# Kernel optimization log

Hardware: AMD Instinct MI355X
Metric: run time of the kernel (lower is better)

Reference implementation:

```python
import jax, jax.numpy as jnp
import numpy as np

N = 50000      # nodes
E = 640000     # edges (before self-loops)
FIN = 512      # in_channels
H = 4          # heads
C = 32         # per-head dim (hidden_channels // heads)
HID = 128      # hidden_channels
OUT = 64       # out_channels
NC = 2         # num_classes


def setup_inputs() -> dict:
    key = jax.random.key(0)
    ks = jax.random.split(key, 26)
    rn = lambda k, shp, s=0.05: jax.random.normal(k, shp, jnp.float32) * s
    return {
        "x": jax.random.normal(ks[0], (N, FIN), jnp.float32),
        "edge_index": jax.random.randint(ks[1], (2, E), 0, N, dtype=jnp.int32),
        "batch": jnp.zeros((N,), jnp.int32),
        # GATConv 1: FIN -> H x C (concat -> HID)
        "W1": rn(ks[2], (FIN, H * C)), "as1": rn(ks[3], (H, C)), "ad1": rn(ks[4], (H, C)), "b1": jnp.zeros((H * C,), jnp.float32),
        "g1": jnp.ones((HID,), jnp.float32), "be1": jnp.zeros((HID,), jnp.float32),
        # GATConv 2: HID -> H x C
        "W2": rn(ks[5], (HID, H * C)), "as2": rn(ks[6], (H, C)), "ad2": rn(ks[7], (H, C)), "b2": jnp.zeros((H * C,), jnp.float32),
        "g2": jnp.ones((HID,), jnp.float32), "be2": jnp.zeros((HID,), jnp.float32),
        "W3": rn(ks[8], (HID, OUT)), "as3": rn(ks[9], (1, OUT)), "ad3": rn(ks[10], (1, OUT)), "b3": jnp.zeros((OUT,), jnp.float32),
        "g3": jnp.ones((OUT,), jnp.float32), "be3": jnp.zeros((OUT,), jnp.float32),
        # classifier: Linear(2*OUT, HID) -> ReLU -> Linear(HID, NC)
        "cW1": rn(ks[11], (2 * OUT, HID)), "cb1": jnp.zeros((HID,), jnp.float32),
        "cW2": rn(ks[12], (HID, NC)), "cb2": jnp.zeros((NC,), jnp.float32),
    }


def _gat_conv(x, ei, W, a_s, a_d, b, heads, cdim, concat):
    n = x.shape[0]
    h = (x @ W).reshape(n, heads, cdim)                 # [n,H,C]
    src, dst = ei[0], ei[1]
    al_s = (h * a_s).sum(-1)                            # [n,H]
    al_d = (h * a_d).sum(-1)                            # [n,H]
    e = al_s[src] + al_d[dst]                           # [E',H]
    e = jnp.where(e > 0, e, 0.2 * e)                    # LeakyReLU(0.2)
    m = jax.ops.segment_max(e, dst, num_segments=n)     # segment softmax over dst
    ex = jnp.exp(e - m[dst])
    s = jax.ops.segment_sum(ex, dst, num_segments=n)
    alpha = ex / (s[dst] + 1e-16)                       # [E',H]
    out = jax.ops.segment_sum(h[src] * alpha[:, :, None], dst, num_segments=n)
    out = out.reshape(n, heads * cdim) if concat else out.mean(axis=1)
    return out + b


def _layer_norm(x, g, b):
    mu = x.mean(-1, keepdims=True)
    v = ((x - mu) ** 2).mean(-1, keepdims=True)
    return g * (x - mu) * jax.lax.rsqrt(v + 1e-5) + b


def reference(x, edge_index, batch, W1, as1, ad1, b1, g1, be1, W2, as2, ad2, b2, g2, be2, W3, as3, ad3, b3, g3, be3, cW1, cb1, cW2, cb2):
    n = x.shape[0]
    ar = jnp.arange(n, dtype=edge_index.dtype)
    ei = jnp.concatenate([edge_index, jnp.stack([ar, ar])], axis=1)  # add self-loops (PyG default)
    h = jax.nn.elu(_layer_norm(_gat_conv(x, ei, W1, as1, ad1, b1, H, C, True), g1, be1))
    h = jax.nn.elu(_layer_norm(_gat_conv(h, ei, W2, as2, ad2, b2, H, C, True), g2, be2))
    h = jax.nn.elu(_layer_norm(_gat_conv(h, ei, W3, as3, ad3, b3, 1, OUT, False), g3, be3))
    # global mean / max pooling over batch ids (single graph here, B=1)
    B = 1
    cnt = jax.ops.segment_sum(jnp.ones((n, 1), h.dtype), batch, num_segments=B)
    x_mean = jax.ops.segment_sum(h, batch, num_segments=B) / cnt
    x_max = jax.ops.segment_max(h, batch, num_segments=B)
    z = jnp.concatenate([x_mean, x_max], axis=-1)       # [B, 2*OUT]
    z = jax.nn.relu(z @ cW1 + cb1)
    return z @ cW2 + cb2                                 # [B, NC]
```

## Files before the change

kernel.cpp:

```cpp
#include <hip/hip_runtime.h>
#include <cmath>

static constexpr int TPB = 256;

using short8 = __attribute__((ext_vector_type(8))) short;
using half8  = __attribute__((ext_vector_type(8))) _Float16;
using f32x4  = __attribute__((ext_vector_type(4))) float;
using uint4v = __attribute__((ext_vector_type(4))) unsigned int;
typedef unsigned short ushort;
typedef unsigned int uint;

__device__ __forceinline__ ushort f2h(float f) {
  _Float16 h = (_Float16)f;
  return __builtin_bit_cast(ushort, h);
}
__device__ __forceinline__ float h2f(ushort u) {
  return (float)__builtin_bit_cast(_Float16, u);
}
__device__ __forceinline__ float hlo(uint u) { return h2f((ushort)(u & 0xffffu)); }
__device__ __forceinline__ float hhi(uint u) { return h2f((ushort)(u >> 16)); }

__global__ void prep_wt3(const float* __restrict__ W1, ushort* __restrict__ Wt1,
                         const float* __restrict__ W2, ushort* __restrict__ Wt2,
                         const float* __restrict__ W3, ushort* __restrict__ Wt3,
                         int FIN) {
  int idx = blockIdx.x * TPB + threadIdx.x;
  const int n1 = FIN * 128, n2 = 128 * 128, n3 = 128 * 64;
  if (idx < n1) {
    int nc = idx / FIN, k = idx - nc * FIN;
    Wt1[idx] = f2h(W1[(size_t)k * 128 + nc]);
  } else if (idx < n1 + n2) {
    int i = idx - n1;
    int nc = i / 128, k = i - nc * 128;
    Wt2[i] = f2h(W2[(size_t)k * 128 + nc]);
  } else if (idx < n1 + n2 + n3) {
    int i = idx - n1 - n2;
    int nc = i / 128, k = i - nc * 128;
    Wt3[i] = f2h(W3[(size_t)k * 64 + nc]);
  }
}

template <int ABF16, int BN, int FUSEMODE>
__global__ __launch_bounds__(256) void gemm_mfma(const void* __restrict__ Ap,
                                                 const ushort* __restrict__ Wt,
                                                 ushort* __restrict__ Cb,
                                                 int n, int K,
                                                 const float* __restrict__ a_s,
                                                 const float* __restrict__ a_d,
                                                 float* __restrict__ als,
                                                 float* __restrict__ ald) {
  constexpr int NF = BN / 32;
  __shared__ short As[64 * 72];
  __shared__ short Bs[BN * 72];
  const int tid = threadIdx.x;
  const int row0 = blockIdx.x * 64;
  const int srow = tid >> 2, sks = (tid & 3) << 4;
  const int wave = tid >> 6, lane = tid & 63;
  const int wr = wave >> 1, wc = wave & 1;
  const int lm = lane & 15, lg = lane >> 4;

  f32x4 acc[2][NF] = {};

  for (int k0 = 0; k0 < K; k0 += 64) {
    {
      int gr = row0 + srow;
      short8 v0 = {0, 0, 0, 0, 0, 0, 0, 0}, v1 = v0;
      if constexpr (ABF16 == 0) {
        const float* A = (const float*)Ap;
        if (gr < n) {
          const float* p = A + (size_t)gr * K + k0 + sks;
          float4 f0 = *(const float4*)(p + 0);
          float4 f1 = *(const float4*)(p + 4);
          float4 f2 = *(const float4*)(p + 8);
          float4 f3 = *(const float4*)(p + 12);
          v0[0] = (short)f2h(f0.x); v0[1] = (short)f2h(f0.y); v0[2] = (short)f2h(f0.z); v0[3] = (short)f2h(f0.w);
          v0[4] = (short)f2h(f1.x); v0[5] = (short)f2h(f1.y); v0[6] = (short)f2h(f1.z); v0[7] = (short)f2h(f1.w);
          v1[0] = (short)f2h(f2.x); v1[1] = (short)f2h(f2.y); v1[2] = (short)f2h(f2.z); v1[3] = (short)f2h(f2.w);
          v1[4] = (short)f2h(f3.x); v1[5] = (short)f2h(f3.y); v1[6] = (short)f2h(f3.z); v1[7] = (short)f2h(f3.w);
        }
      } else {
        const ushort* A = (const ushort*)Ap;
        if (gr < n) {
          const ushort* p = A + (size_t)gr * K + k0 + sks;
          v0 = *(const short8*)(p + 0);
          v1 = *(const short8*)(p + 8);
        }
      }
      *(short8*)&As[srow * 72 + sks + 0] = v0;
      *(short8*)&As[srow * 72 + sks + 8] = v1;
    }
    if constexpr (BN == 128) {
      const int brow = tid >> 1, bks = (tid & 1) << 5;
      const ushort* wp = Wt + (size_t)brow * K + k0 + bks;
      *(short8*)&Bs[brow * 72 + bks + 0]  = *(const short8*)(wp + 0);
      *(short8*)&Bs[brow * 72 + bks + 8]  = *(const short8*)(wp + 8);
      *(short8*)&Bs[brow * 72 + bks + 16] = *(const short8*)(wp + 16);
      *(short8*)&Bs[brow * 72 + bks + 24] = *(const short8*)(wp + 24);
    } else {
      const ushort* wp = Wt + (size_t)srow * K + k0 + sks;
      *(short8*)&Bs[srow * 72 + sks + 0] = *(const short8*)(wp + 0);
      *(short8*)&Bs[srow * 72 + sks + 8] = *(const short8*)(wp + 8);
    }
    __syncthreads();
#pragma unroll
    for (int kk = 0; kk < 64; kk += 32) {
      half8 a0 = *(const half8*)&As[(wr * 32 + lm) * 72 + kk + lg * 8];
      half8 a1 = *(const half8*)&As[(wr * 32 + 16 + lm) * 72 + kk + lg * 8];
      half8 bf[NF];
#pragma unroll
      for (int f = 0; f < NF; ++f)
        bf[f] = *(const half8*)&Bs[(wc * (BN / 2) + f * 16 + lm) * 72 + kk + lg * 8];
#pragma unroll
      for (int f = 0; f < NF; ++f) {
        acc[0][f] = __builtin_amdgcn_mfma_f32_16x16x32_f16(a0, bf[f], acc[0][f], 0, 0, 0);
        acc[1][f] = __builtin_amdgcn_mfma_f32_16x16x32_f16(a1, bf[f], acc[1][f], 0, 0, 0);
      }
    }
    __syncthreads();
  }
#pragma unroll
  for (int m = 0; m < 2; ++m)
#pragma unroll
    for (int f = 0; f < NF; ++f)
#pragma unroll
      for (int r = 0; r < 4; ++r) {
        int row = row0 + wr * 32 + m * 16 + lg * 4 + r;
        if (row < n) {
          int col = wc * (BN / 2) + f * 16 + lm;
          Cb[(size_t)row * BN + col] = f2h(acc[m][f][r]);
        }
      }
  if constexpr (FUSEMODE == 1) {
#pragma unroll
    for (int hh = 0; hh < 2; ++hh) {
      const int head = 2 * wc + hh;
      float as0 = a_s[head * 32 + lm], as1 = a_s[head * 32 + 16 + lm];
      float ad0 = a_d[head * 32 + lm], ad1 = a_d[head * 32 + 16 + lm];
#pragma unroll
      for (int m = 0; m < 2; ++m)
#pragma unroll
        for (int r = 0; r < 4; ++r) {
          float tS = acc[m][2 * hh][r] * as0 + acc[m][2 * hh + 1][r] * as1;
          float tD = acc[m][2 * hh][r] * ad0 + acc[m][2 * hh + 1][r] * ad1;
#pragma unroll
          for (int off = 8; off >= 1; off >>= 1) {
            tS += __shfl_xor(tS, off);
            tD += __shfl_xor(tD, off);
          }
          if (lm == 0) {
            int row = row0 + wr * 32 + m * 16 + lg * 4 + r;
            if (row < n) {
              als[(size_t)row * 4 + head] = tS;
              ald[(size_t)row * 4 + head] = tD;
            }
          }
        }
    }
  }
  if constexpr (FUSEMODE == 2) {
    float* alsp = (float*)As;
    float* aldp = alsp + 64;
    float tS[2][4], tD[2][4];
#pragma unroll
    for (int m = 0; m < 2; ++m)
#pragma unroll
      for (int r = 0; r < 4; ++r) {
        int col0c = wc * 32;
        float s = acc[m][0][r] * a_s[col0c + lm] + acc[m][1][r] * a_s[col0c + 16 + lm];
        float dd = acc[m][0][r] * a_d[col0c + lm] + acc[m][1][r] * a_d[col0c + 16 + lm];
#pragma unroll
        for (int off = 8; off >= 1; off >>= 1) {
          s += __shfl_xor(s, off);
          dd += __shfl_xor(dd, off);
        }
        tS[m][r] = s;
        tD[m][r] = dd;
      }
    if (wc == 0) {
#pragma unroll
      for (int m = 0; m < 2; ++m)
#pragma unroll
        for (int r = 0; r < 4; ++r)
          if (lm == 0) {
            int rl = wr * 32 + m * 16 + lg * 4 + r;
            alsp[rl] = tS[m][r];
            aldp[rl] = tD[m][r];
          }
    }
    __syncthreads();
    if (wc == 1) {
#pragma unroll
      for (int m = 0; m < 2; ++m)
#pragma unroll
        for (int r = 0; r < 4; ++r)
          if (lm == 0) {
            int rl = wr * 32 + m * 16 + lg * 4 + r;
            int row = row0 + rl;
            if (row < n) {
              als[row] = alsp[rl] + tS[m][r];
              ald[row] = aldp[rl] + tD[m][r];
            }
          }
    }
  }
}

__global__ void zero_int(int* __restrict__ p, int n) {
  int i = blockIdx.x * TPB + threadIdx.x;
  if (i < n) p[i] = 0;
}

__global__ void hist_dst(const int* __restrict__ edst, int* __restrict__ counts,
                         int E0, int Et) {
  int e = blockIdx.x * TPB + threadIdx.x;
  if (e >= Et) return;
  int d = e < E0 ? edst[e] : e - E0;
  atomicAdd(&counts[d], 1);
}

__global__ void block_sums(const int* __restrict__ counts, int* __restrict__ bsum, int N) {
  __shared__ int sh[256];
  int t = threadIdx.x, idx = blockIdx.x * 256 + t;
  sh[t] = idx < N ? counts[idx] : 0;
  __syncthreads();
  for (int off = 128; off >= 1; off >>= 1) {
    if (t < off) sh[t] += sh[t + off];
    __syncthreads();
  }
  if (t == 0) bsum[blockIdx.x] = sh[0];
}

__global__ void scan_bsum(int* __restrict__ bsum, int nb) {
  __shared__ int sh[256];
  int t = threadIdx.x;
  int v = t < nb ? bsum[t] : 0;
  sh[t] = v;
  __syncthreads();
  for (int off = 1; off < 256; off <<= 1) {
    int u = (t >= off) ? sh[t - off] : 0;
    __syncthreads();
    sh[t] += u;
    __syncthreads();
  }
  if (t < nb) bsum[t] = sh[t] - v;
}

__global__ void scan_final(const int* __restrict__ counts, const int* __restrict__ bsum_ex,
                           int* __restrict__ offsets, int* __restrict__ cursor,
                           int N, int Et) {
  __shared__ int sh[256];
  int t = threadIdx.x, b = blockIdx.x;
  int idx = b * 256 + t;
  int v = (idx < N) ? counts[idx] : 0;
  sh[t] = v;
  __syncthreads();
  for (int off = 1; off < 256; off <<= 1) {
    int u = (t >= off) ? sh[t - off] : 0;
    __syncthreads();
    sh[t] += u;
    __syncthreads();
  }
  if (idx < N) {
    int o = bsum_ex[b] + sh[t] - v;
    offsets[idx] = o;
    cursor[idx] = o;
  }
  if (idx == 0) offsets[N] = Et;
}

__global__ void scatter_csr(const int* __restrict__ esrc, const int* __restrict__ edst,
                            int* __restrict__ cursor, int* __restrict__ csr_src,
                            int E0, int Et) {
  int e = blockIdx.x * TPB + threadIdx.x;
  if (e >= Et) return;
  int s = e < E0 ? esrc[e] : e - E0;
  int d = e < E0 ? edst[e] : e - E0;
  int pos = atomicAdd(&cursor[d], 1);
  csr_src[pos] = s;
}

template <int HH, int CC>
__global__ __launch_bounds__(256) void fused_attn(
    const ushort* __restrict__ hb, const float* __restrict__ als,
    const float* __restrict__ ald, const int* __restrict__ offsets,
    const int* __restrict__ csr_src, const float* __restrict__ bias,
    const float* __restrict__ g, const float* __restrict__ be,
    ushort* __restrict__ xout, int n) {
  constexpr int W = HH * CC;
  constexpr int LPE = W / 8;
  constexpr int NEG = 64 / LPE;
  int wid = (int)((blockIdx.x * (size_t)blockDim.x + threadIdx.x) >> 6);
  int lane = threadIdx.x & 63;
  if (wid >= n) return;
  const int d = wid;
  const int begin = offsets[d], end = offsets[d + 1];
  const int deg = end - begin;

  const int grp = lane / LPE, sub = lane % LPE;
  const int c0 = sub * 8;

  float acc[8] = {};

  if (HH == 4 && deg <= 16) {
    const int h16 = lane >> 4, j16 = lane & 15;
    bool act = j16 < deg;
    int s_e = csr_src[begin + (act ? j16 : 0)];
    float e;
    {
      float ad_h = ald[(size_t)d * 4 + h16];
      e = act ? (als[(size_t)s_e * 4 + h16] + ad_h) : -1e30f;
      e = e > 0.f ? e : 0.2f * e;
    }
    float m = e;
#pragma unroll
    for (int off = 8; off >= 1; off >>= 1) m = fmaxf(m, __shfl_xor(m, off));
    float p = act ? __expf(e - m) : 0.f;
    float s = p;
#pragma unroll
    for (int off = 8; off >= 1; off >>= 1) s += __shfl_xor(s, off);
    float alpha = p / (s + 1e-16f);

    const int hc = sub >> 2;
    int j = grp;
    int sj = __shfl(s_e, j & 15);
    uint4v u = *(const uint4v*)(hb + (size_t)sj * W + c0);
    for (int j0 = 0; j0 < deg; j0 += NEG) {
      uint4v ucur = u;
      int jcur = j;
      j += NEG;
      if (j0 + NEG < deg) {
        int sn = __shfl(s_e, j & 15);
        u = *(const uint4v*)(hb + (size_t)sn * W + c0);
      }
      float w = __shfl(alpha, (hc << 4) | (jcur & 15));
#pragma unroll
      for (int i = 0; i < 4; ++i) {
        acc[2 * i]     = fmaf(w, hlo(ucur[i]), acc[2 * i]);
        acc[2 * i + 1] = fmaf(w, hhi(ucur[i]), acc[2 * i + 1]);
      }
    }
  } else {

  const int hsel = sub >> 2;
  float aldv[HH];
  if constexpr (HH == 4) {
    float4 t = *(const float4*)(ald + (size_t)d * 4);
    aldv[0] = t.x; aldv[1] = t.y; aldv[2] = t.z; aldv[3] = t.w;
  } else {
    aldv[0] = ald[d];
  }

  auto sel4 = [&](float x0, float x1, float x2, float x3) {
    float lo = (hsel & 1) ? x1 : x0;
    float hi = (hsel & 1) ? x3 : x2;
    return (hsel & 2) ? hi : lo;
  };

  if (deg <= 64) {
    bool act = lane < deg;
    int s_e = act ? csr_src[begin + lane] : 0;
    float e0 = -1e30f, e1 = -1e30f, e2 = -1e30f, e3 = -1e30f;
    if constexpr (HH == 4) {
      if (act) {
        float4 t = *(const float4*)(als + (size_t)s_e * 4);
        e0 = t.x + aldv[0]; e0 = e0 > 0.f ? e0 : 0.2f * e0;
        e1 = t.y + aldv[1]; e1 = e1 > 0.f ? e1 : 0.2f * e1;
        e2 = t.z + aldv[2]; e2 = e2 > 0.f ? e2 : 0.2f * e2;
        e3 = t.w + aldv[3]; e3 = e3 > 0.f ? e3 : 0.2f * e3;
      }
    } else {
      if (act) {
        e0 = als[s_e] + aldv[0]; e0 = e0 > 0.f ? e0 : 0.2f * e0;
      }
    }
    float m0 = e0, m1 = e1, m2 = e2, m3 = e3;
#pragma unroll
    for (int off = 32; off >= 1; off >>= 1) {
      m0 = fmaxf(m0, __shfl_xor(m0, off));
      if constexpr (HH == 4) {
        m1 = fmaxf(m1, __shfl_xor(m1, off));
        m2 = fmaxf(m2, __shfl_xor(m2, off));
        m3 = fmaxf(m3, __shfl_xor(m3, off));
      }
    }
    float p0 = act ? __expf(e0 - m0) : 0.f;
    float p1 = 0.f, p2 = 0.f, p3 = 0.f;
    if constexpr (HH == 4) {
      p1 = act ? __expf(e1 - m1) : 0.f;
      p2 = act ? __expf(e2 - m2) : 0.f;
      p3 = act ? __expf(e3 - m3) : 0.f;
    }
    float s0 = p0, s1 = p1, s2 = p2, s3 = p3;
#pragma unroll
    for (int off = 32; off >= 1; off >>= 1) {
      s0 += __shfl_xor(s0, off);
      if constexpr (HH == 4) {
        s1 += __shfl_xor(s1, off);
        s2 += __shfl_xor(s2, off);
        s3 += __shfl_xor(s3, off);
      }
    }
    float a0 = p0 / (s0 + 1e-16f);
    float a1 = 0.f, a2 = 0.f, a3 = 0.f;
    if constexpr (HH == 4) {
      a1 = p1 / (s1 + 1e-16f);
      a2 = p2 / (s2 + 1e-16f);
      a3 = p3 / (s3 + 1e-16f);
    }

    int j = grp;
    int sj = __shfl(s_e, j < 64 ? j : 0);
    uint4v u = *(const uint4v*)(hb + (size_t)sj * W + c0);
    for (int j0 = 0; j0 < deg; j0 += NEG) {
      uint4v ucur = u;
      int jcur = j;
      j += NEG;
      if (j0 + NEG < deg) {
        int sn = __shfl(s_e, j < 64 ? j : 0);
        u = *(const uint4v*)(hb + (size_t)sn * W + c0);
      }
      int jc = jcur < 64 ? jcur : 0;
      float w;
      if constexpr (HH == 4) {
        float wa = __shfl(a0, jc), wb = __shfl(a1, jc), wcx = __shfl(a2, jc), wd = __shfl(a3, jc);
        w = sel4(wa, wb, wcx, wd);
      } else {
        w = __shfl(a0, jc);
      }
      if (jcur >= deg) w = 0.f;
#pragma unroll
      for (int i = 0; i < 4; ++i) {
        acc[2 * i]     = fmaf(w, hlo(ucur[i]), acc[2 * i]);
        acc[2 * i + 1] = fmaf(w, hhi(ucur[i]), acc[2 * i + 1]);
      }
    }
  } else {
    float me[HH];
#pragma unroll
    for (int h = 0; h < HH; ++h) me[h] = -1e30f;
    for (int k = begin + lane; k < end; k += 64) {
      int s = csr_src[k];
      if constexpr (HH == 4) {
        float4 t = *(const float4*)(als + (size_t)s * 4);
        float e0 = t.x + aldv[0]; e0 = e0 > 0.f ? e0 : 0.2f * e0; me[0] = fmaxf(me[0], e0);
        float e1 = t.y + aldv[1]; e1 = e1 > 0.f ? e1 : 0.2f * e1; me[1] = fmaxf(me[1], e1);
        float e2 = t.z + aldv[2]; e2 = e2 > 0.f ? e2 : 0.2f * e2; me[2] = fmaxf(me[2], e2);
        float e3 = t.w + aldv[3]; e3 = e3 > 0.f ? e3 : 0.2f * e3; me[3] = fmaxf(me[3], e3);
      } else {
        float e0 = als[s] + aldv[0]; e0 = e0 > 0.f ? e0 : 0.2f * e0; me[0] = fmaxf(me[0], e0);
      }
    }
#pragma unroll
    for (int off = 32; off >= 1; off >>= 1)
#pragma unroll
      for (int h = 0; h < HH; ++h) me[h] = fmaxf(me[h], __shfl_xor(me[h], off));
    float se[HH];
#pragma unroll
    for (int h = 0; h < HH; ++h) se[h] = 0.f;
    for (int k = begin + lane; k < end; k += 64) {
      int s = csr_src[k];
      if constexpr (HH == 4) {
        float4 t = *(const float4*)(als + (size_t)s * 4);
        float e0 = t.x + aldv[0]; e0 = e0 > 0.f ? e0 : 0.2f * e0; se[0] += __expf(e0 - me[0]);
        float e1 = t.y + aldv[1]; e1 = e1 > 0.f ? e1 : 0.2f * e1; se[1] += __expf(e1 - me[1]);
        float e2 = t.z + aldv[2]; e2 = e2 > 0.f ? e2 : 0.2f * e2; se[2] += __expf(e2 - me[2]);
        float e3 = t.w + aldv[3]; e3 = e3 > 0.f ? e3 : 0.2f * e3; se[3] += __expf(e3 - me[3]);
      } else {
        float e0 = als[s] + aldv[0]; e0 = e0 > 0.f ? e0 : 0.2f * e0; se[0] += __expf(e0 - me[0]);
      }
    }
#pragma unroll
    for (int off = 32; off >= 1; off >>= 1)
#pragma unroll
      for (int h = 0; h < HH; ++h) se[h] += __shfl_xor(se[h], off);
    float inv[HH];
#pragma unroll
    for (int h = 0; h < HH; ++h) inv[h] = 1.f / (se[h] + 1e-16f);

    float m_my, i_my, ad_my;
    if constexpr (HH == 4) {
      m_my = sel4(me[0], me[1], me[2], me[3]);
      i_my = sel4(inv[0], inv[1], inv[2], inv[3]);
      ad_my = sel4(aldv[0], aldv[1], aldv[2], aldv[3]);
    } else {
      m_my = me[0]; i_my = inv[0]; ad_my = aldv[0];
    }
    for (int j0 = 0; j0 < deg; j0 += NEG) {
      int j = j0 + grp;
      if (j < deg) {
        int s = csr_src[begin + j];
        float as_my;
        if constexpr (HH == 4) {
          float4 t = *(const float4*)(als + (size_t)s * 4);
          as_my = sel4(t.x, t.y, t.z, t.w);
        } else {
          as_my = als[s];
        }
        float e = as_my + ad_my; e = e > 0.f ? e : 0.2f * e;
        float w = __expf(e - m_my) * i_my;
        uint4v u = *(const uint4v*)(hb + (size_t)s * W + c0);
#pragma unroll
        for (int i = 0; i < 4; ++i) {
          acc[2 * i]     = fmaf(w, hlo(u[i]), acc[2 * i]);
          acc[2 * i + 1] = fmaf(w, hhi(u[i]), acc[2 * i + 1]);
        }
      }
    }
  }
  }

#pragma unroll
  for (int i = 0; i < 8; ++i) {
    if constexpr (HH == 1) acc[i] += __shfl_xor(acc[i], 8);
    acc[i] += __shfl_xor(acc[i], 16);
    acc[i] += __shfl_xor(acc[i], 32);
  }

  float4 bv0 = *(const float4*)(bias + c0);
  float4 bv1 = *(const float4*)(bias + c0 + 4);
  float v[8];
  v[0] = acc[0] + bv0.x; v[1] = acc[1] + bv0.y; v[2] = acc[2] + bv0.z; v[3] = acc[3] + bv0.w;
  v[4] = acc[4] + bv1.x; v[5] = acc[5] + bv1.y; v[6] = acc[6] + bv1.z; v[7] = acc[7] + bv1.w;
  float sm = 0.f, s2 = 0.f;
#pragma unroll
  for (int i = 0; i < 8; ++i) { sm += v[i]; s2 += v[i] * v[i]; }
  constexpr int TOPOFF = LPE / 2;
#pragma unroll
  for (int off = TOPOFF; off >= 1; off >>= 1) {
    sm += __shfl_xor(sm, off);
    s2 += __shfl_xor(s2, off);
  }
  const float invW = 1.0f / W;
  float mu = sm * invW;
  float var = s2 * invW - mu * mu;
  float r = rsqrtf(var + 1e-5f);
  float4 gv0 = *(const float4*)(g + c0);
  float4 gv1 = *(const float4*)(g + c0 + 4);
  float4 be0 = *(const float4*)(be + c0);
  float4 be1 = *(const float4*)(be + c0 + 4);
  float gg[8] = {gv0.x, gv0.y, gv0.z, gv0.w, gv1.x, gv1.y, gv1.z, gv1.w};
  float bb[8] = {be0.x, be0.y, be0.z, be0.w, be1.x, be1.y, be1.z, be1.w};
  uint4v pk;
#pragma unroll
  for (int i = 0; i < 4; ++i) {
    float y0 = gg[2 * i] * (v[2 * i] - mu) * r + bb[2 * i];
    y0 = y0 > 0.f ? y0 : __expf(y0) - 1.f;
    float y1 = gg[2 * i + 1] * (v[2 * i + 1] - mu) * r + bb[2 * i + 1];
    y1 = y1 > 0.f ? y1 : __expf(y1) - 1.f;
    pk[i] = (uint)f2h(y0) | ((uint)f2h(y1) << 16);
  }
  if (grp == 0)
    *(uint4v*)(xout + (size_t)wid * W + c0) = pk;
}

__global__ void pool_partial(const ushort* __restrict__ h, float* __restrict__ psum,
                             float* __restrict__ pmax, int n) {
  int tid = threadIdx.x;
  float lsum = 0.f, lmax = -1e30f;
  for (size_t idx = (size_t)blockIdx.x * 256 + tid; idx < (size_t)n * 64;
       idx += (size_t)gridDim.x * 256) {
    float v = h2f(h[idx]);
    lsum += v;
    lmax = fmaxf(lmax, v);
  }
  __shared__ float ss[256], sm[256];
  ss[tid] = lsum; sm[tid] = lmax;
  __syncthreads();
  if (tid < 64) {
    float a = ss[tid] + ss[tid + 64] + ss[tid + 128] + ss[tid + 192];
    float m = fmaxf(fmaxf(sm[tid], sm[tid + 64]), fmaxf(sm[tid + 128], sm[tid + 192]));
    psum[blockIdx.x * 64 + tid] = a;
    pmax[blockIdx.x * 64 + tid] = m;
  }
}

__global__ __launch_bounds__(256) void pool_final(
    const float* __restrict__ psum, const float* __restrict__ pmax,
    int nblocks, int n, const float* __restrict__ cW1,
    const float* __restrict__ cb1, const float* __restrict__ cW2,
    const float* __restrict__ cb2, float* __restrict__ out) {
  __shared__ float sred[4][64], mred[4][64];
  __shared__ float z[128];
  __shared__ float hid[128];
  int tid = threadIdx.x;
  int c = tid & 63, q = tid >> 6;
  float s = 0.f, m = -1e30f;
  for (int b = q; b < nblocks; b += 4) {
    s += psum[b * 64 + c];
    m = fmaxf(m, pmax[b * 64 + c]);
  }
  sred[q][c] = s; mred[q][c] = m;
  __syncthreads();
  if (q == 0) {
    float st = sred[0][c] + sred[1][c] + sred[2][c] + sred[3][c];
    float mt = fmaxf(fmaxf(mred[0][c], mred[1][c]), fmaxf(mred[2][c], mred[3][c]));
    z[c] = st / (float)n;
    z[64 + c] = mt;
  }
  __syncthreads();
  if (tid < 128) {
    float a = cb1[tid];
#pragma unroll 4
    for (int k = 0; k < 128; ++k) a += z[k] * cW1[k * 128 + tid];
    hid[tid] = fmaxf(a, 0.f);
  }
  __syncthreads();
  if (tid < 2) {
    float o = cb2[tid];
    for (int j = 0; j < 128; ++j) o += hid[j] * cW2[j * 2 + tid];
    out[tid] = o;
  }
}

static inline int cdiv(long long a, long long b) { return (int)((a + b - 1) / b); }

extern "C" void kernel_launch(void* const* d_in, const int* in_sizes, int n_in,
                              void* d_out, int out_size, void* d_ws, size_t ws_size,
                              hipStream_t stream) {
  const float* x   = (const float*)d_in[0];
  const int*   ei  = (const int*)d_in[1];
  const float* W1  = (const float*)d_in[3];
  const float* as1 = (const float*)d_in[4];
  const float* ad1 = (const float*)d_in[5];
  const float* b1  = (const float*)d_in[6];
  const float* g1  = (const float*)d_in[7];
  const float* be1 = (const float*)d_in[8];
  const float* W2  = (const float*)d_in[9];
  const float* as2 = (const float*)d_in[10];
  const float* ad2 = (const float*)d_in[11];
  const float* b2  = (const float*)d_in[12];
  const float* g2  = (const float*)d_in[13];
  const float* be2 = (const float*)d_in[14];
  const float* W3  = (const float*)d_in[15];
  const float* as3 = (const float*)d_in[16];
  const float* ad3 = (const float*)d_in[17];
  const float* b3  = (const float*)d_in[18];
  const float* g3  = (const float*)d_in[19];
  const float* be3 = (const float*)d_in[20];
  const float* cW1 = (const float*)d_in[21];
  const float* cb1 = (const float*)d_in[22];
  const float* cW2 = (const float*)d_in[23];
  const float* cb2 = (const float*)d_in[24];
  float* out = (float*)d_out;

  const int N   = in_sizes[2];
  const int E0  = in_sizes[1] / 2;
  const int Et  = E0 + N;
  const int FIN = in_sizes[0] / N;

  float* ws = (float*)d_ws;
  size_t o = 0;
  ushort* Ab = (ushort*)(ws + o); o += (size_t)N * 64;
  ushort* Bb = (ushort*)(ws + o); o += (size_t)N * 64;
  float* als  = ws + o; o += (size_t)N * 4;
  float* ald  = ws + o; o += (size_t)N * 4;
  ushort* Wt1 = (ushort*)(ws + o); o += (128 * 512) / 2;
  ushort* Wt2 = (ushort*)(ws + o); o += (128 * 128) / 2;
  ushort* Wt3 = (ushort*)(ws + o); o += (64 * 128) / 2;
  float* psum = ws + o; o += 64 * 64;
  float* pmax = ws + o; o += 64 * 64;
  int* counts  = (int*)(ws + o); o += N + 1;
  int* offsets = (int*)(ws + o); o += N + 1;
  int* cursor  = (int*)(ws + o); o += N;
  int* bsum    = (int*)(ws + o); o += 256;
  int* csr_src = (int*)(ws + o); o += Et;

  const int* esrc = ei;
  const int* edst = ei + E0;
  const int NB = cdiv(N, 256);

  prep_wt3<<<cdiv((long long)FIN * 128 + 128 * 128 + 128 * 64, TPB), TPB, 0, stream>>>(
      W1, Wt1, W2, Wt2, W3, Wt3, FIN);

  zero_int<<<cdiv(N + 1, TPB), TPB, 0, stream>>>(counts, N + 1);
  hist_dst<<<cdiv(Et, TPB), TPB, 0, stream>>>(edst, counts, E0, Et);
  block_sums<<<NB, 256, 0, stream>>>(counts, bsum, N);
  scan_bsum<<<1, 256, 0, stream>>>(bsum, NB);
  scan_final<<<NB, 256, 0, stream>>>(counts, bsum, offsets, cursor, N, Et);
  scatter_csr<<<cdiv(Et, TPB), TPB, 0, stream>>>(esrc, edst, cursor, csr_src, E0, Et);

  gemm_mfma<0, 128, 1><<<cdiv(N, 64), 256, 0, stream>>>(x, Wt1, Ab, N, FIN, as1, ad1, als, ald);
  fused_attn<4, 32><<<cdiv(N, 4), 256, 0, stream>>>(Ab, als, ald, offsets, csr_src, b1, g1, be1, Bb, N);
  gemm_mfma<1, 128, 1><<<cdiv(N, 64), 256, 0, stream>>>(Bb, Wt2, Ab, N, 128, as2, ad2, als, ald);
  fused_attn<4, 32><<<cdiv(N, 4), 256, 0, stream>>>(Ab, als, ald, offsets, csr_src, b2, g2, be2, Bb, N);
  gemm_mfma<1, 64, 2><<<cdiv(N, 64), 256, 0, stream>>>(Bb, Wt3, Ab, N, 128, as3, ad3, als, ald);
  fused_attn<1, 64><<<cdiv(N, 4), 256, 0, stream>>>(Ab, als, ald, offsets, csr_src, b3, g3, be3, Bb, N);
  pool_partial<<<64, 256, 0, stream>>>(Bb, psum, pmax, N);
  pool_final<<<1, 256, 0, stream>>>(psum, pmax, 64, N, cW1, cb1, cW2, cb2, out);
}
```

Before: 320.6 us.

## Double-buffer shared-memory tiles in MFMA GEMM with register prefetch

The GEMM kernel now keeps two LDS buffers for the A and B tiles. It loads the next K-tile from global memory into registers while MFMAs run on the current tile, then writes it into the other buffer. This hides global load latency and removes one barrier per K step, at the cost of doubled LDS use and extra live registers, which may lower occupancy. A barrier is added before FUSEMODE 2 reuses the A buffer as scratch.

```diff
diff --git a/kernel.cpp b/kernel.cpp
--- a/kernel.cpp
+++ b/kernel.cpp
@@ -50,73 +50,110 @@
                                                  float* __restrict__ als,
                                                  float* __restrict__ ald) {
   constexpr int NF = BN / 32;
-  __shared__ short As[64 * 72];
-  __shared__ short Bs[BN * 72];
+  __shared__ short As[2][64 * 72];
+  __shared__ short Bs[2][BN * 72];
   const int tid = threadIdx.x;
   const int row0 = blockIdx.x * 64;
   const int srow = tid >> 2, sks = (tid & 3) << 4;
+  const int brow = tid >> 1, bks = (tid & 1) << 5;
   const int wave = tid >> 6, lane = tid & 63;
   const int wr = wave >> 1, wc = wave & 1;
   const int lm = lane & 15, lg = lane >> 4;
 
   f32x4 acc[2][NF] = {};
 
-  for (int k0 = 0; k0 < K; k0 += 64) {
-    {
-      int gr = row0 + srow;
-      short8 v0 = {0, 0, 0, 0, 0, 0, 0, 0}, v1 = v0;
-      if constexpr (ABF16 == 0) {
-        const float* A = (const float*)Ap;
-        if (gr < n) {
-          const float* p = A + (size_t)gr * K + k0 + sks;
-          float4 f0 = *(const float4*)(p + 0);
-          float4 f1 = *(const float4*)(p + 4);
-          float4 f2 = *(const float4*)(p + 8);
-          float4 f3 = *(const float4*)(p + 12);
-          v0[0] = (short)f2h(f0.x); v0[1] = (short)f2h(f0.y); v0[2] = (short)f2h(f0.z); v0[3] = (short)f2h(f0.w);
-          v0[4] = (short)f2h(f1.x); v0[5] = (short)f2h(f1.y); v0[6] = (short)f2h(f1.z); v0[7] = (short)f2h(f1.w);
-          v1[0] = (short)f2h(f2.x); v1[1] = (short)f2h(f2.y); v1[2] = (short)f2h(f2.z); v1[3] = (short)f2h(f2.w);
-          v1[4] = (short)f2h(f3.x); v1[5] = (short)f2h(f3.y); v1[6] = (short)f2h(f3.z); v1[7] = (short)f2h(f3.w);
-        }
-      } else {
-        const ushort* A = (const ushort*)Ap;
-        if (gr < n) {
-          const ushort* p = A + (size_t)gr * K + k0 + sks;
-          v0 = *(const short8*)(p + 0);
-          v1 = *(const short8*)(p + 8);
-        }
-      }
-      *(short8*)&As[srow * 72 + sks + 0] = v0;
-      *(short8*)&As[srow * 72 + sks + 8] = v1;
+  float4 fa0, fa1, fa2, fa3;
+  short8 sa0, sa1;
+  short8 sb0, sb1, sb2, sb3;
+  bool arow_ok;
+
+  auto LOADT = [&](int k0) {
+    int gr = row0 + srow;
+    arow_ok = gr < n;
+    if constexpr (ABF16 == 0) {
+      const float* A = (const float*)Ap;
+      if (arow_ok) {
+        const float* p = A + (size_t)gr * K + k0 + sks;
+        fa0 = *(const float4*)(p + 0);
+        fa1 = *(const float4*)(p + 4);
+        fa2 = *(const float4*)(p + 8);
+        fa3 = *(const float4*)(p + 12);
+      }
+    } else {
+      const ushort* A = (const ushort*)Ap;
+      if (arow_ok) {
+        const ushort* p = A + (size_t)gr * K + k0 + sks;
+        sa0 = *(const short8*)(p + 0);
+        sa1 = *(const short8*)(p + 8);
+      }
     }
     if constexpr (BN == 128) {
-      const int brow = tid >> 1, bks = (tid & 1) << 5;
       const ushort* wp = Wt + (size_t)brow * K + k0 + bks;
-      *(short8*)&Bs[brow * 72 + bks + 0]  = *(const short8*)(wp + 0);
-      *(short8*)&Bs[brow * 72 + bks + 8]  = *(const short8*)(wp + 8);
-      *(short8*)&Bs[brow * 72 + bks + 16] = *(const short8*)(wp + 16);
-      *(short8*)&Bs[brow * 72 + bks + 24] = *(const short8*)(wp + 24);
+      sb0 = *(const short8*)(wp + 0);
+      sb1 = *(const short8*)(wp + 8);
+      sb2 = *(const short8*)(wp + 16);
+      sb3 = *(const short8*)(wp + 24);
     } else {
       const ushort* wp = Wt + (size_t)srow * K + k0 + sks;
-      *(short8*)&Bs[srow * 72 + sks + 0] = *(const short8*)(wp + 0);
-      *(short8*)&Bs[srow * 72 + sks + 8] = *(const short8*)(wp + 8);
-    }
-    __syncthreads();
+      sb0 = *(const short8*)(wp + 0);
+      sb1 = *(const short8*)(wp + 8);
+    }
+  };
+  auto WRITET = [&](int b) {
+    short8 w0, w1;
+    if constexpr (ABF16 == 0) {
+      short8 z = {0, 0, 0, 0, 0, 0, 0, 0};
+      w0 = z; w1 = z;
+      if (arow_ok) {
+        w0[0] = (short)f2h(fa0.x); w0[1] = (short)f2h(fa0.y); w0[2] = (short)f2h(fa0.z); w0[3] = (short)f2h(fa0.w);
+        w0[4] = (short)f2h(fa1.x); w0[5] = (short)f2h(fa1.y); w0[6] = (short)f2h(fa1.z); w0[7] = (short)f2h(fa1.w);
+        w1[0] = (short)f2h(fa2.x); w1[1] = (short)f2h(fa2.y); w1[2] = (short)f2h(fa2.z); w1[3] = (short)f2h(fa2.w);
+        w1[4] = (short)f2h(fa3.x); w1[5] = (short)f2h(fa3.y); w1[6] = (short)f2h(fa3.z); w1[7] = (short)f2h(fa3.w);
+      }
+    } else {
+      short8 z = {0, 0, 0, 0, 0, 0, 0, 0};
+      w0 = arow_ok ? sa0 : z;
+      w1 = arow_ok ? sa1 : z;
+    }
+    *(short8*)&As[b][srow * 72 + sks + 0] = w0;
+    *(short8*)&As[b][srow * 72 + sks + 8] = w1;
+    if constexpr (BN == 128) {
+      *(short8*)&Bs[b][brow * 72 + bks + 0]  = sb0;
+      *(short8*)&Bs[b][brow * 72 + bks + 8]  = sb1;
+      *(short8*)&Bs[b][brow * 72 + bks + 16] = sb2;
+      *(short8*)&Bs[b][brow * 72 + bks + 24] = sb3;
+    } else {
+      *(short8*)&Bs[b][srow * 72 + sks + 0] = sb0;
+      *(short8*)&Bs[b][srow * 72 + sks + 8] = sb1;
+    }
+  };
+
+  LOADT(0);
+  WRITET(0);
+  __syncthreads();
+  const int nk = K >> 6;
+  for (int t = 0; t < nk; ++t) {
+    const int cur = t & 1;
+    const bool more = (t + 1) < nk;
+    if (more) LOADT((t + 1) << 6);
 #pragma unroll
     for (int kk = 0; kk < 64; kk += 32) {
-      half8 a0 = *(const half8*)&As[(wr * 32 + lm) * 72 + kk + lg * 8];
-      half8 a1 = *(const half8*)&As[(wr * 32 + 16 + lm) * 72 + kk + lg * 8];
+      half8 a0 = *(const half8*)&As[cur][(wr * 32 + lm) * 72 + kk + lg * 8];
+      half8 a1 = *(const half8*)&As[cur][(wr * 32 + 16 + lm) * 72 + kk + lg * 8];
       half8 bf[NF];
 #pragma unroll
       for (int f = 0; f < NF; ++f)
-        bf[f] = *(const half8*)&Bs[(wc * (BN / 2) + f * 16 + lm) * 72 + kk + lg * 8];
+        bf[f] = *(const half8*)&Bs[cur][(wc * (BN / 2) + f * 16 + lm) * 72 + kk + lg * 8];
 #pragma unroll
       for (int f = 0; f < NF; ++f) {
         acc[0][f] = __builtin_amdgcn_mfma_f32_16x16x32_f16(a0, bf[f], acc[0][f], 0, 0, 0);
         acc[1][f] = __builtin_amdgcn_mfma_f32_16x16x32_f16(a1, bf[f], acc[1][f], 0, 0, 0);
       }
     }
-    __syncthreads();
+    if (more) {
+      WRITET(cur ^ 1);
+      __syncthreads();
+    }
   }
 #pragma unroll
   for (int m = 0; m < 2; ++m)
@@ -158,7 +195,8 @@
     }
   }
   if constexpr (FUSEMODE == 2) {
-    float* alsp = (float*)As;
+    __syncthreads();
+    float* alsp = (float*)&As[0][0];
     float* aldp = alsp + 64;
     float tS[2][4], tD[2][4];
 #pragma unroll
```

After: 324.8 us. No clear change (+1.3%).
